# Kernel optimization log

Hardware: AMD Instinct MI355X
Metric: run time of the kernel (lower is better)

## Reference

```python
import jax, jax.numpy as jnp
import numpy as np

N, IN_F, OUT_F, H = 4096, 256, 512, 8
D = OUT_F // H  # hidden per head
NEG_SLOPE = 0.2


def setup_inputs() -> dict:
    key = jax.random.key(0)
    k1, k2, k3 = jax.random.split(key, 3)
    inp = jax.random.normal(k1, (N, IN_F), dtype=jnp.float32)
    A = jnp.zeros((N, N), dtype=jnp.float32)  # additive adjacency mask
    # xavier_uniform for W [out, in]
    limW = float(np.sqrt(6.0 / (IN_F + H * D)))
    W = jax.random.uniform(k2, (H * D, IN_F), minval=-limW, maxval=limW, dtype=jnp.float32)
    lima = float(np.sqrt(6.0 / (H * D + 1)))
    a_left = jax.random.uniform(k3, (1, H, D), minval=-lima, maxval=lima, dtype=jnp.float32)
    return {"inp": inp, "A": A, "W": W, "a_left": a_left}


def reference(inp, A, W, a_left):
    # h: [N, H, D]
    h = (inp @ W.T).reshape(-1, H, D)
    # NOTE: source uses a_left for BOTH source and target scores (a_right is dead code)
    scores = jnp.sum(h * a_left, axis=-1)  # [N, H]
    s = scores.T  # [H, N]
    # [H, N, N] additive attention logits
    logits = jax.nn.leaky_relu(s[:, :, None] + s[:, None, :], negative_slope=NEG_SLOPE)
    logits = logits + A[None, :, :]
    att = jax.nn.softmax(logits, axis=-1)  # [H, N, N]
    # bmm: [H,N,N] x [H,N,D] -> [H,N,D] -> [N,H,D]
    out = jnp.einsum('hij,jhd->ihd', att, h)
    return out.reshape(-1, H * D)
```

## Files before the change

### kernel.cpp

```cpp
#include <hip/hip_runtime.h>
#include <math.h>

#define N 4096
#define IN_F 256
#define OUT_F 512
#define H 8
#define D 64
#define NEG 0.2f
#define JC 1024

typedef __attribute__((ext_vector_type(8))) short bf16x8;
typedef __attribute__((ext_vector_type(4))) float f32x4;

__device__ __forceinline__ float leaky(float x) { return fmaxf(x, NEG * x); }

__device__ __forceinline__ unsigned short f2bf(float x) {
    union { float f; unsigned u; } v; v.f = x;
    unsigned r = v.u + 0x7fff + ((v.u >> 16) & 1);
    return (unsigned short)(r >> 16);
}

__device__ __forceinline__ unsigned fmap(float x) {
    union { float f; unsigned u; } v; v.f = x;
    return (v.u & 0x80000000u) ? ~v.u : (v.u | 0x80000000u);
}
__device__ __forceinline__ float funmap(unsigned m) {
    union { float f; unsigned u; } v;
    v.u = (m & 0x80000000u) ? (m & 0x7fffffffu) : ~m;
    return v.f;
}

__device__ __forceinline__ void dma16(const void* g, void* l) {
    __builtin_amdgcn_global_load_lds((const __attribute__((address_space(1))) void*)g,
                                     (__attribute__((address_space(3))) void*)l, 16, 0, 0);
}

__global__ __launch_bounds__(256, 4) void k_gemm(const float* __restrict__ inp,
                                                 const float* __restrict__ W,
                                                 const float* __restrict__ a_left,
                                                 unsigned short* __restrict__ hbT,
                                                 float* __restrict__ s,
                                                 unsigned* __restrict__ smaxU) {
    __shared__ float As[64][36];
    __shared__ float Bs[64][68];
    __shared__ unsigned short h_st[32][72];
    __shared__ float s_red[32];

    const int t = threadIdx.x;
    const int bi = blockIdx.x;
    const int head = blockIdx.y;
    const int iy = t >> 4, ox = t & 15;
    const int iA = t >> 3, kA = (t & 7) * 8;
    const int oB = t >> 2, kB = (t & 3) * 16;

    float4 pa[2], pb[4];
    auto loadrk = [&](int k0) {
        const float* ip = &inp[(size_t)(bi * 32 + iA) * IN_F + k0 + kA];
        const float* wp = &W[(size_t)(head * 64 + oB) * IN_F + k0 + kB];
#pragma unroll
        for (int q = 0; q < 2; ++q) pa[q] = *(const float4*)&ip[q * 4];
#pragma unroll
        for (int q = 0; q < 4; ++q) pb[q] = *(const float4*)&wp[q * 4];
    };
    loadrk(0);

    float acc[2][4] = {};
    for (int k0 = 0; k0 < IN_F; k0 += 64) {
        __syncthreads();
#pragma unroll
        for (int q = 0; q < 2; ++q)
#pragma unroll
            for (int j = 0; j < 4; ++j) As[kA + q * 4 + j][iA] = ((const float*)&pa[q])[j];
#pragma unroll
        for (int q = 0; q < 4; ++q)
#pragma unroll
            for (int j = 0; j < 4; ++j) Bs[kB + q * 4 + j][oB] = ((const float*)&pb[q])[j];
        __syncthreads();
        if (k0 + 64 < IN_F) loadrk(k0 + 64);
#pragma unroll
        for (int k = 0; k < 64; ++k) {
            float2 a2 = *(const float2*)&As[k][iy * 2];
            float4 b4 = *(const float4*)&Bs[k][ox * 4];
            float a[2] = {a2.x, a2.y};
            float b[4] = {b4.x, b4.y, b4.z, b4.w};
#pragma unroll
            for (int r = 0; r < 2; ++r)
#pragma unroll
                for (int c = 0; c < 4; ++c) acc[r][c] = fmaf(a[r], b[c], acc[r][c]);
        }
    }

    float aL[4];
#pragma unroll
    for (int c = 0; c < 4; ++c) aL[c] = a_left[head * D + ox * 4 + c];
#pragma unroll
    for (int r = 0; r < 2; ++r) {
        float sp = acc[r][0] * aL[0] + acc[r][1] * aL[1] + acc[r][2] * aL[2] + acc[r][3] * aL[3];
        sp += __shfl_xor(sp, 1); sp += __shfl_xor(sp, 2);
        sp += __shfl_xor(sp, 4); sp += __shfl_xor(sp, 8);
        if (ox == 0) {
            s[head * N + bi * 32 + iy * 2 + r] = sp;
            s_red[iy * 2 + r] = sp;
        }
    }
    __syncthreads();
    if (t < 32) {
        float m = s_red[t];
        for (int off = 16; off; off >>= 1) m = fmaxf(m, __shfl_down(m, off, 64));
        if (t == 0) atomicMax(&smaxU[head], fmap(m));
    }

#pragma unroll
    for (int r = 0; r < 2; ++r) {
        ushort4 v;
        v.x = f2bf(acc[r][0]); v.y = f2bf(acc[r][1]);
        v.z = f2bf(acc[r][2]); v.w = f2bf(acc[r][3]);
        *(ushort4*)&h_st[iy * 2 + r][ox * 4] = v;
    }
    __syncthreads();
    {
        const int d = t >> 2, iq = (t & 3) * 8;
        unsigned short us[8];
#pragma unroll
        for (int k = 0; k < 8; ++k) us[k] = h_st[iq + k][d];
        unsigned short* dst = &hbT[((size_t)(head * D + d)) * N + bi * 32 + iq];
#pragma unroll
        for (int q = 0; q < 2; ++q) {
            ushort4 v = {us[q * 4 + 0], us[q * 4 + 1], us[q * 4 + 2], us[q * 4 + 3]};
            *(ushort4*)&dst[q * 4] = v;
        }
    }
}

__global__ __launch_bounds__(256) void k_prep(const float* __restrict__ A,
                                              unsigned short* __restrict__ Abf,
                                              float* __restrict__ rmax) {
    int i = blockIdx.x;
    const float* row = &A[(size_t)i * N];
    unsigned short* dst = &Abf[(size_t)i * N];
    float m = -1e30f;
    for (int j = threadIdx.x * 4; j < N; j += 256 * 4) {
        float4 v = *(const float4*)&row[j];
        m = fmaxf(fmaxf(fmaxf(m, v.x), fmaxf(v.y, v.z)), v.w);
        ushort4 b = {f2bf(v.x), f2bf(v.y), f2bf(v.z), f2bf(v.w)};
        *(ushort4*)&dst[j] = b;
    }
    for (int off = 32; off; off >>= 1) m = fmaxf(m, __shfl_down(m, off, 64));
    __shared__ float red[4];
    if ((threadIdx.x & 63) == 0) red[threadIdx.x >> 6] = m;
    __syncthreads();
    if (threadIdx.x == 0) rmax[i] = fmaxf(fmaxf(red[0], red[1]), fmaxf(red[2], red[3]));
}

__global__ __launch_bounds__(256) void k_rowmax(const float* __restrict__ A,
                                                float* __restrict__ rmax) {
    int i = blockIdx.x;
    const float* row = &A[(size_t)i * N];
    float m = -1e30f;
    for (int j = threadIdx.x * 4; j < N; j += 256 * 4) {
        float4 v = *(const float4*)&row[j];
        m = fmaxf(fmaxf(fmaxf(m, v.x), fmaxf(v.y, v.z)), v.w);
    }
    for (int off = 32; off; off >>= 1) m = fmaxf(m, __shfl_down(m, off, 64));
    __shared__ float red[4];
    if ((threadIdx.x & 63) == 0) red[threadIdx.x >> 6] = m;
    __syncthreads();
    if (threadIdx.x == 0) rmax[i] = fmaxf(fmaxf(red[0], red[1]), fmaxf(red[2], red[3]));
}

__device__ __forceinline__ int swz(int r) { return (r ^ (r >> 2)) & 3; }

__global__ __launch_bounds__(256, 4) void k_attn_big(const unsigned short* __restrict__ Abf,
                                                     const unsigned short* __restrict__ hbT,
                                                     const float* __restrict__ s,
                                                     const unsigned* __restrict__ smaxU,
                                                     const float* __restrict__ rmax,
                                                     float* __restrict__ out,
                                                     float* __restrict__ Z) {
    __shared__ unsigned short A_st[2][128 * 32];
    __shared__ unsigned short hT_st[2][64 * 32];
    __shared__ float s_ch[JC];

    const int t = threadIdx.x;
    const int i0 = blockIdx.x * 128;
    const int head = blockIdx.y;
    const int j0 = blockIdx.z * JC;
    const int lane = t & 63, wave = t >> 6, quad = lane >> 4, li = lane & 15;

    *(float4*)&s_ch[t * 4] = *(const float4*)&s[head * N + j0 + t * 4];

    const float smx = funmap(smaxU[head]);
    float s_i[2], negmb[2];
#pragma unroll
    for (int is = 0; is < 2; ++is) {
        int row = i0 + wave * 32 + is * 16 + li;
        float sv = s[head * N + row];
        s_i[is] = sv;
        negmb[is] = -(leaky(sv + smx) + rmax[row]);
    }

    const unsigned short* gA[2]; unsigned short* lA[2][2];
#pragma unroll
    for (int q = 0; q < 2; ++q) {
        int slot = q * 256 + t, row = slot >> 2, u = slot & 3;
        gA[q] = Abf + (size_t)(i0 + row) * N + j0 + ((u ^ swz(row)) << 3);
        lA[0][q] = &A_st[0][slot * 8];
        lA[1][q] = &A_st[1][slot * 8];
    }
    const unsigned short* gH; unsigned short* lH[2];
    {
        int slot = t, d = slot >> 2, u = slot & 3;
        gH = hbT + (size_t)head * D * N + (size_t)d * N + j0 + ((u ^ swz(d)) << 3);
        lH[0] = &hT_st[0][slot * 8];
        lH[1] = &hT_st[1][slot * 8];
    }

    f32x4 acc[2][4] = {};
    f32x4 accz[2] = {};
    bf16x8 onesb;
#pragma unroll
    for (int i = 0; i < 8; ++i) onesb[i] = 0x3F80;

#pragma unroll
    for (int q = 0; q < 2; ++q) dma16(gA[q], lA[0][q]);
    dma16(gH, lH[0]);

    for (int tt = 0; tt < JC / 32; ++tt) {
        const int p = tt & 1;
        __syncthreads();
        if (tt + 1 < JC / 32) {
            const int ju = (tt + 1) * 32;
#pragma unroll
            for (int q = 0; q < 2; ++q) dma16(gA[q] + ju, lA[p ^ 1][q]);
            dma16(gH + ju, lH[p ^ 1]);
        }
        const int jt = tt * 32;

        float4 s0 = *(const float4*)&s_ch[jt + quad * 8];
        float4 s1 = *(const float4*)&s_ch[jt + quad * 8 + 4];
        float sv[8] = {s0.x, s0.y, s0.z, s0.w, s1.x, s1.y, s1.z, s1.w};
        bf16x8 hf[4];
#pragma unroll
        for (int db = 0; db < 4; ++db) {
            int d = db * 16 + li;
            hf[db] = *(const bf16x8*)&hT_st[p][(d * 4 + (quad ^ swz(d))) * 8];
        }
#pragma unroll
        for (int is = 0; is < 2; ++is) {
            int r = wave * 32 + is * 16 + li;
            uint4 au = *(const uint4*)&A_st[p][(r * 4 + (quad ^ swz(r))) * 8];
            unsigned auv[4] = {au.x, au.y, au.z, au.w};
            union { bf16x8 v; unsigned u[4]; } P;
            const float si = s_i[is], nmb = negmb[is];
#pragma unroll
            for (int w = 0; w < 4; ++w) {
                float aLo = __uint_as_float(auv[w] << 16);
                float aHi = __uint_as_float(auv[w] & 0xffff0000u);
                float t0 = si + sv[2 * w], t1 = si + sv[2 * w + 1];
                float l0 = fmaxf(t0, NEG * t0), l1 = fmaxf(t1, NEG * t1);
                float e0 = __expf(l0 + (aLo + nmb));
                float e1 = __expf(l1 + (aHi + nmb));
                unsigned r0 = __float_as_uint(e0) + 0x8000u;
                unsigned r1 = __float_as_uint(e1) + 0x8000u;
                P.u[w] = __builtin_amdgcn_perm(r1, r0, 0x07060302u);
            }
#pragma unroll
            for (int db = 0; db < 4; ++db)
                acc[is][db] = __builtin_amdgcn_mfma_f32_16x16x32_bf16(P.v, hf[db], acc[is][db], 0, 0, 0);
            accz[is] = __builtin_amdgcn_mfma_f32_16x16x32_bf16(P.v, onesb, accz[is], 0, 0, 0);
        }
    }

#pragma unroll
    for (int is = 0; is < 2; ++is) {
        int rowbase = i0 + wave * 32 + is * 16 + quad * 4;
#pragma unroll
        for (int r = 0; r < 4; ++r) {
            float* op = &out[(size_t)(rowbase + r) * OUT_F + head * D];
#pragma unroll
            for (int db = 0; db < 4; ++db) atomicAdd(&op[db * 16 + li], acc[is][db][r]);
        }
        if (li == 0) {
#pragma unroll
            for (int r = 0; r < 4; ++r) atomicAdd(&Z[head * N + rowbase + r], accz[is][r]);
        }
    }
}

#define JCF 2048
__global__ __launch_bounds__(256, 4) void k_attn_f(const float* __restrict__ A,
                                                   const unsigned short* __restrict__ hbT,
                                                   const float* __restrict__ s,
                                                   const unsigned* __restrict__ smaxU,
                                                   const float* __restrict__ rmax,
                                                   float* __restrict__ out,
                                                   float* __restrict__ Z) {
    __shared__ float A_stf[64 * 16 * 4];
    __shared__ unsigned short hT_stf[64 * 8 * 8];
    __shared__ float s_ch[JCF];

    const int t = threadIdx.x;
    const int i0 = blockIdx.x * 64;
    const int head = blockIdx.y;
    const int j0 = blockIdx.z * JCF;
    const int lane = t & 63, wave = t >> 6, quad = lane >> 4, li = lane & 15;
    const int iw = wave * 16;
    const int myrow = i0 + iw + li;

#pragma unroll
    for (int q = 0; q < 2; ++q) {
        int idx = q * 256 + t;
        *(float4*)&s_ch[idx * 4] = *(const float4*)&s[head * N + j0 + idx * 4];
    }
    const float s_i = s[head * N + myrow];
    const float mb = leaky(s_i + funmap(smaxU[head])) + rmax[myrow];

    const float* gA[4]; void* lA[4];
#pragma unroll
    for (int q = 0; q < 4; ++q) {
        int slot = q * 256 + t;
        int r = slot >> 4, c4p = slot & 15;
        int c4 = c4p ^ (r & 7);
        gA[q] = &A[(size_t)(i0 + r) * N + j0 + c4 * 4];
        lA[q] = (void*)&A_stf[slot * 4];
    }
    const unsigned short* gH[2]; void* lH[2];
#pragma unroll
    for (int q = 0; q < 2; ++q) {
        int slot = q * 256 + t;
        int r = slot >> 3, u = slot & 7;
        int uc = u ^ (r & 7);
        gH[q] = &hbT[(size_t)head * D * N + (size_t)r * N + j0 + uc * 8];
        lH[q] = (void*)&hT_stf[slot * 8];
    }

    f32x4 acc[4] = {{0, 0, 0, 0}, {0, 0, 0, 0}, {0, 0, 0, 0}, {0, 0, 0, 0}};
    float zsum = 0.f;

    for (int jt = 0; jt < JCF; jt += 64) {
        __syncthreads();
#pragma unroll
        for (int q = 0; q < 4; ++q) dma16(gA[q] + jt, lA[q]);
#pragma unroll
        for (int q = 0; q < 2; ++q) dma16(gH[q] + jt, lH[q]);
        __syncthreads();

#pragma unroll
        for (int kh = 0; kh < 2; ++kh) {
            const int u0 = kh * 8 + quad * 2;
            const int sw = li & 7;
            float4 a0 = *(const float4*)&A_stf[((iw + li) * 16 + (u0 ^ sw)) * 4];
            float4 a1 = *(const float4*)&A_stf[((iw + li) * 16 + ((u0 + 1) ^ sw)) * 4];
            const int jl = kh * 32 + quad * 8;
            float4 s0 = *(const float4*)&s_ch[jt + jl];
            float4 s1 = *(const float4*)&s_ch[jt + jl + 4];
            float av[8] = {a0.x, a0.y, a0.z, a0.w, a1.x, a1.y, a1.z, a1.w};
            float sv[8] = {s0.x, s0.y, s0.z, s0.w, s1.x, s1.y, s1.z, s1.w};
            union { bf16x8 v; unsigned u[4]; } P;
#pragma unroll
            for (int p = 0; p < 4; ++p) {
                float x0 = s_i + sv[2 * p + 0];
                float x1 = s_i + sv[2 * p + 1];
                float w0 = __expf(fmaxf(x0, NEG * x0) + (av[2 * p + 0] - mb));
                float w1 = __expf(fmaxf(x1, NEG * x1) + (av[2 * p + 1] - mb));
                zsum += w0 + w1;
                P.u[p] = ((unsigned)f2bf(w1) << 16) | (unsigned)f2bf(w0);
            }
#pragma unroll
            for (int db = 0; db < 4; ++db) {
                int slotH = (db * 16 + li) * 8 + ((kh * 4 + quad) ^ sw);
                bf16x8 hf = *(const bf16x8*)&hT_stf[slotH * 8];
                acc[db] = __builtin_amdgcn_mfma_f32_16x16x32_bf16(P.v, hf, acc[db], 0, 0, 0);
            }
        }
    }

    zsum += __shfl_xor(zsum, 16);
    zsum += __shfl_xor(zsum, 32);
    if (quad == 0) atomicAdd(&Z[head * N + myrow], zsum);

#pragma unroll
    for (int r = 0; r < 4; ++r) {
        float* op = &out[(size_t)(i0 + iw + quad * 4 + r) * OUT_F + head * D];
#pragma unroll
        for (int db = 0; db < 4; ++db) atomicAdd(&op[db * 16 + li], acc[db][r]);
    }
}

__global__ __launch_bounds__(256) void k_norm(float* __restrict__ out,
                                              const float* __restrict__ Z) {
    int idx = blockIdx.x * 256 + threadIdx.x;
    int i = idx >> 9, hd = idx & 511, hh = hd >> 6;
    out[idx] = out[idx] / Z[hh * N + i];
}

extern "C" void kernel_launch(void* const* d_in, const int* in_sizes, int n_in,
                              void* d_out, int out_size, void* d_ws, size_t ws_size,
                              hipStream_t stream) {
    const float* inp = (const float*)d_in[0];
    const float* A = (const float*)d_in[1];
    const float* W = (const float*)d_in[2];
    const float* a_left = (const float*)d_in[3];
    float* out = (float*)d_out;

    unsigned short* hbT = (unsigned short*)d_ws;
    float* s = (float*)((char*)d_ws + (size_t)H * D * N * 2);
    float* Z = s + (size_t)H * N;
    unsigned* smaxU = (unsigned*)(Z + (size_t)H * N);
    float* rmax = (float*)(smaxU + 8);
    unsigned short* Abf = (unsigned short*)((char*)d_ws + ((size_t)5 << 20));
    const bool big = ws_size >= (((size_t)5 << 20) + (size_t)N * N * 2);

    hipMemsetAsync(out, 0, (size_t)N * OUT_F * sizeof(float), stream);
    hipMemsetAsync(Z, 0, (size_t)H * N * sizeof(float) + 8 * sizeof(unsigned), stream);

    k_gemm<<<dim3(N / 32, H), 256, 0, stream>>>(inp, W, a_left, hbT, s, smaxU);
    if (big) {
        k_prep<<<dim3(N), 256, 0, stream>>>(A, Abf, rmax);
        k_attn_big<<<dim3(N / 128, H, N / JC), 256, 0, stream>>>(Abf, hbT, s, smaxU, rmax, out, Z);
    } else {
        k_rowmax<<<dim3(N), 256, 0, stream>>>(A, rmax);
        k_attn_f<<<dim3(N / 64, H, N / JCF), 256, 0, stream>>>(A, hbT, s, smaxU, rmax, out, Z);
    }
    k_norm<<<dim3(N * OUT_F / 256), 256, 0, stream>>>(out, Z);
}
```

Before: 215.3 us.

## Use split-bf16 MFMA for projection GEMM and drop LDS staging in attention

The fp32 input projection GEMM is replaced by an MFMA kernel using a hi/lo bf16 split (three MFMAs per tile) to keep near-fp32 accuracy. The split conversion of inp and W is folded into the A-prep kernel. The attention kernel drops its LDS double-buffered DMA staging and reads A and h fragments directly from global memory into registers. This trades LDS traffic and barriers for uncoalesced-ish global reads that depend on cache hits, and adds workspace for the split copies.

```diff
diff --git a/kernel.cpp b/kernel.cpp
--- a/kernel.cpp
+++ b/kernel.cpp
@@ -19,6 +19,9 @@
     unsigned r = v.u + 0x7fff + ((v.u >> 16) & 1);
     return (unsigned short)(r >> 16);
 }
+__device__ __forceinline__ float bf2f(unsigned short b) {
+    union { float f; unsigned u; } v; v.u = ((unsigned)b) << 16; return v.f;
+}
 
 __device__ __forceinline__ unsigned fmap(float x) {
     union { float f; unsigned u; } v; v.f = x;
@@ -35,12 +38,238 @@
                                      (__attribute__((address_space(3))) void*)l, 16, 0, 0);
 }
 
-__global__ __launch_bounds__(256, 4) void k_gemm(const float* __restrict__ inp,
-                                                 const float* __restrict__ W,
-                                                 const float* __restrict__ a_left,
-                                                 unsigned short* __restrict__ hbT,
-                                                 float* __restrict__ s,
-                                                 unsigned* __restrict__ smaxU) {
+
+__global__ __launch_bounds__(256) void k_prep(const float* __restrict__ A,
+                                              const float* __restrict__ inp,
+                                              const float* __restrict__ W,
+                                              unsigned short* __restrict__ Abf,
+                                              float* __restrict__ rmax,
+                                              unsigned short* __restrict__ inpH,
+                                              unsigned short* __restrict__ inpL,
+                                              unsigned short* __restrict__ WH,
+                                              unsigned short* __restrict__ WL) {
+    const int i = blockIdx.x, t = threadIdx.x;
+    const float* row = &A[(size_t)i * N];
+    unsigned short* dst = &Abf[(size_t)i * N];
+    float m = -1e30f;
+    for (int j = t * 4; j < N; j += 256 * 4) {
+        float4 v = *(const float4*)&row[j];
+        m = fmaxf(fmaxf(fmaxf(m, v.x), fmaxf(v.y, v.z)), v.w);
+        ushort4 b = {f2bf(v.x), f2bf(v.y), f2bf(v.z), f2bf(v.w)};
+        *(ushort4*)&dst[j] = b;
+    }
+    for (int off = 32; off; off >>= 1) m = fmaxf(m, __shfl_down(m, off, 64));
+    __shared__ float red[4];
+    if ((t & 63) == 0) red[t >> 6] = m;
+    __syncthreads();
+    if (t == 0) rmax[i] = fmaxf(fmaxf(red[0], red[1]), fmaxf(red[2], red[3]));
+
+    {
+        float v = inp[(size_t)i * IN_F + t];
+        unsigned short hi = f2bf(v);
+        inpH[(size_t)i * IN_F + t] = hi;
+        inpL[(size_t)i * IN_F + t] = f2bf(v - bf2f(hi));
+    }
+    if (i < OUT_F) {
+        float v = W[(size_t)i * IN_F + t];
+        unsigned short hi = f2bf(v);
+        WH[(size_t)i * IN_F + t] = hi;
+        WL[(size_t)i * IN_F + t] = f2bf(v - bf2f(hi));
+    }
+}
+
+__global__ __launch_bounds__(256) void k_gemm(const unsigned short* __restrict__ inpH,
+                                              const unsigned short* __restrict__ inpL,
+                                              const unsigned short* __restrict__ WH,
+                                              const unsigned short* __restrict__ WL,
+                                              const float* __restrict__ a_left,
+                                              unsigned short* __restrict__ hbT,
+                                              float* __restrict__ s,
+                                              unsigned* __restrict__ smaxU) {
+    __shared__ unsigned short h_st[64][72];
+    __shared__ float s_red[64];
+    const int t = threadIdx.x, bx = blockIdx.x, head = blockIdx.y;
+    const int wave = t >> 6, lane = t & 63, quad = lane >> 4, li = lane & 15;
+    const int i0 = bx * 64;
+
+    const unsigned short* pAH = inpH + (size_t)(i0 + wave * 16 + li) * IN_F + quad * 8;
+    const unsigned short* pAL = inpL + (size_t)(i0 + wave * 16 + li) * IN_F + quad * 8;
+    const unsigned short* pBH[4];
+    const unsigned short* pBL[4];
+#pragma unroll
+    for (int ot = 0; ot < 4; ++ot) {
+        pBH[ot] = WH + (size_t)(head * 64 + ot * 16 + li) * IN_F + quad * 8;
+        pBL[ot] = WL + (size_t)(head * 64 + ot * 16 + li) * IN_F + quad * 8;
+    }
+
+    f32x4 acc[4] = {};
+#pragma unroll
+    for (int ks = 0; ks < 8; ++ks) {
+        bf16x8 ah = *(const bf16x8*)(pAH + ks * 32);
+        bf16x8 al = *(const bf16x8*)(pAL + ks * 32);
+#pragma unroll
+        for (int ot = 0; ot < 4; ++ot) {
+            bf16x8 bh = *(const bf16x8*)(pBH[ot] + ks * 32);
+            bf16x8 bl = *(const bf16x8*)(pBL[ot] + ks * 32);
+            acc[ot] = __builtin_amdgcn_mfma_f32_16x16x32_bf16(ah, bh, acc[ot], 0, 0, 0);
+            acc[ot] = __builtin_amdgcn_mfma_f32_16x16x32_bf16(al, bh, acc[ot], 0, 0, 0);
+            acc[ot] = __builtin_amdgcn_mfma_f32_16x16x32_bf16(ah, bl, acc[ot], 0, 0, 0);
+        }
+    }
+
+    float aLv[4];
+#pragma unroll
+    for (int ot = 0; ot < 4; ++ot) aLv[ot] = a_left[head * D + ot * 16 + li];
+#pragma unroll
+    for (int r = 0; r < 4; ++r) {
+        float sp = acc[0][r] * aLv[0] + acc[1][r] * aLv[1] + acc[2][r] * aLv[2] + acc[3][r] * aLv[3];
+        sp += __shfl_xor(sp, 1); sp += __shfl_xor(sp, 2);
+        sp += __shfl_xor(sp, 4); sp += __shfl_xor(sp, 8);
+        if (li == 0) {
+            int rloc = wave * 16 + quad * 4 + r;
+            s[head * N + i0 + rloc] = sp;
+            s_red[rloc] = sp;
+        }
+    }
+#pragma unroll
+    for (int ot = 0; ot < 4; ++ot)
+#pragma unroll
+        for (int r = 0; r < 4; ++r)
+            h_st[wave * 16 + quad * 4 + r][ot * 16 + li] = f2bf(acc[ot][r]);
+    __syncthreads();
+    if (t < 64) {
+        float m = s_red[t];
+        for (int off = 32; off; off >>= 1) m = fmaxf(m, __shfl_down(m, off, 64));
+        if (t == 0) atomicMax(&smaxU[head], fmap(m));
+    }
+    {
+        const int d = t >> 2, iq = (t & 3) * 16;
+        unsigned short us[16];
+#pragma unroll
+        for (int k = 0; k < 16; ++k) us[k] = h_st[iq + k][d];
+        unsigned short* dst = &hbT[((size_t)(head * D + d)) * N + i0 + iq];
+#pragma unroll
+        for (int q = 0; q < 4; ++q) {
+            ushort4 v = {us[q * 4 + 0], us[q * 4 + 1], us[q * 4 + 2], us[q * 4 + 3]};
+            *(ushort4*)&dst[q * 4] = v;
+        }
+    }
+}
+
+__global__ __launch_bounds__(256, 4) void k_attn(const unsigned short* __restrict__ Abf,
+                                                 const unsigned short* __restrict__ hbT,
+                                                 const float* __restrict__ s,
+                                                 const unsigned* __restrict__ smaxU,
+                                                 const float* __restrict__ rmax,
+                                                 float* __restrict__ out,
+                                                 float* __restrict__ Z) {
+    __shared__ float s_ch[JC];
+
+    const int t = threadIdx.x;
+    const int i0 = blockIdx.x * 128;
+    const int head = blockIdx.y;
+    const int j0 = blockIdx.z * JC;
+    const int lane = t & 63, wave = t >> 6, quad = lane >> 4, li = lane & 15;
+
+    *(float4*)&s_ch[t * 4] = *(const float4*)&s[head * N + j0 + t * 4];
+
+    const float smx = funmap(smaxU[head]);
+    float s_i[2], nmb[2];
+#pragma unroll
+    for (int is = 0; is < 2; ++is) {
+        int row = i0 + wave * 32 + is * 16 + li;
+        float sv = s[head * N + row];
+        s_i[is] = sv;
+        nmb[is] = -(leaky(sv + smx) + rmax[row]);
+    }
+    __syncthreads();
+
+    const unsigned short* pA[2];
+#pragma unroll
+    for (int is = 0; is < 2; ++is)
+        pA[is] = Abf + (size_t)(i0 + wave * 32 + is * 16 + li) * N + j0 + quad * 8;
+    const unsigned short* pH[4];
+#pragma unroll
+    for (int db = 0; db < 4; ++db)
+        pH[db] = hbT + (size_t)(head * D + db * 16 + li) * N + j0 + quad * 8;
+
+    f32x4 acc[2][4] = {};
+    f32x4 accz[2] = {};
+    bf16x8 onesb;
+#pragma unroll
+    for (int i = 0; i < 8; ++i) onesb[i] = 0x3F80;
+
+    for (int tg = 0; tg < JC / 128; ++tg) {
+#pragma unroll
+        for (int u = 0; u < 4; ++u) {
+            bf16x8 hf[4];
+#pragma unroll
+            for (int db = 0; db < 4; ++db) hf[db] = *(const bf16x8*)(pH[db] + u * 32);
+            uint4 au[2];
+#pragma unroll
+            for (int is = 0; is < 2; ++is) au[is] = *(const uint4*)(pA[is] + u * 32);
+            float4 s0 = *(const float4*)&s_ch[tg * 128 + u * 32 + quad * 8];
+            float4 s1 = *(const float4*)&s_ch[tg * 128 + u * 32 + quad * 8 + 4];
+            float sv[8] = {s0.x, s0.y, s0.z, s0.w, s1.x, s1.y, s1.z, s1.w};
+#pragma unroll
+            for (int is = 0; is < 2; ++is) {
+                unsigned auv[4] = {au[is].x, au[is].y, au[is].z, au[is].w};
+                union { bf16x8 v; unsigned u[4]; } P;
+                const float si = s_i[is], nm = nmb[is];
+#pragma unroll
+                for (int w = 0; w < 4; ++w) {
+                    float aLo = __uint_as_float(auv[w] << 16);
+                    float aHi = __uint_as_float(auv[w] & 0xffff0000u);
+                    float x0 = si + sv[2 * w + 0];
+                    float x1 = si + sv[2 * w + 1];
+                    float l0 = fmaxf(x0, NEG * x0);
+                    float l1 = fmaxf(x1, NEG * x1);
+                    float e0 = __expf(l0 + (aLo + nm));
+                    float e1 = __expf(l1 + (aHi + nm));
+                    unsigned r0 = __float_as_uint(e0) + 0x8000u;
+                    unsigned r1 = __float_as_uint(e1) + 0x8000u;
+                    P.u[w] = __builtin_amdgcn_perm(r1, r0, 0x07060302u);
+                }
+#pragma unroll
+                for (int db = 0; db < 4; ++db)
+                    acc[is][db] = __builtin_amdgcn_mfma_f32_16x16x32_bf16(P.v, hf[db], acc[is][db], 0, 0, 0);
+                accz[is] = __builtin_amdgcn_mfma_f32_16x16x32_bf16(P.v, onesb, accz[is], 0, 0, 0);
+            }
+        }
+        pA[0] += 128; pA[1] += 128;
+        pH[0] += 128; pH[1] += 128; pH[2] += 128; pH[3] += 128;
+    }
+
+#pragma unroll
+    for (int is = 0; is < 2; ++is) {
+        int rowbase = i0 + wave * 32 + is * 16 + quad * 4;
+#pragma unroll
+        for (int r = 0; r < 4; ++r) {
+            float* op = &out[(size_t)(rowbase + r) * OUT_F + head * D];
+#pragma unroll
+            for (int db = 0; db < 4; ++db) atomicAdd(&op[db * 16 + li], acc[is][db][r]);
+        }
+        if (li == 0) {
+#pragma unroll
+            for (int r = 0; r < 4; ++r) atomicAdd(&Z[head * N + rowbase + r], accz[is][r]);
+        }
+    }
+}
+
+__global__ __launch_bounds__(256) void k_norm(float* __restrict__ out,
+                                              const float* __restrict__ Z) {
+    int idx = blockIdx.x * 256 + threadIdx.x;
+    int i = idx >> 9, hd = idx & 511, hh = hd >> 6;
+    out[idx] = out[idx] / Z[hh * N + i];
+}
+
+
+__global__ __launch_bounds__(256, 4) void k_gemm_f(const float* __restrict__ inp,
+                                                   const float* __restrict__ W,
+                                                   const float* __restrict__ a_left,
+                                                   unsigned short* __restrict__ hbT,
+                                                   float* __restrict__ s,
+                                                   unsigned* __restrict__ smaxU) {
     __shared__ float As[64][36];
     __shared__ float Bs[64][68];
     __shared__ unsigned short h_st[32][72];
@@ -89,7 +318,6 @@
                 for (int c = 0; c < 4; ++c) acc[r][c] = fmaf(a[r], b[c], acc[r][c]);
         }
     }
-
     float aL[4];
 #pragma unroll
     for (int c = 0; c < 4; ++c) aL[c] = a_left[head * D + ox * 4 + c];
@@ -109,7 +337,6 @@
         for (int off = 16; off; off >>= 1) m = fmaxf(m, __shfl_down(m, off, 64));
         if (t == 0) atomicMax(&smaxU[head], fmap(m));
     }
-
 #pragma unroll
     for (int r = 0; r < 2; ++r) {
         ushort4 v;
@@ -130,26 +357,6 @@
             *(ushort4*)&dst[q * 4] = v;
         }
     }
-}
-
-__global__ __launch_bounds__(256) void k_prep(const float* __restrict__ A,
-                                              unsigned short* __restrict__ Abf,
-                                              float* __restrict__ rmax) {
-    int i = blockIdx.x;
-    const float* row = &A[(size_t)i * N];
-    unsigned short* dst = &Abf[(size_t)i * N];
-    float m = -1e30f;
-    for (int j = threadIdx.x * 4; j < N; j += 256 * 4) {
-        float4 v = *(const float4*)&row[j];
-        m = fmaxf(fmaxf(fmaxf(m, v.x), fmaxf(v.y, v.z)), v.w);
-        ushort4 b = {f2bf(v.x), f2bf(v.y), f2bf(v.z), f2bf(v.w)};
-        *(ushort4*)&dst[j] = b;
-    }
-    for (int off = 32; off; off >>= 1) m = fmaxf(m, __shfl_down(m, off, 64));
-    __shared__ float red[4];
-    if ((threadIdx.x & 63) == 0) red[threadIdx.x >> 6] = m;
-    __syncthreads();
-    if (threadIdx.x == 0) rmax[i] = fmaxf(fmaxf(red[0], red[1]), fmaxf(red[2], red[3]));
 }
 
 __global__ __launch_bounds__(256) void k_rowmax(const float* __restrict__ A,
@@ -166,125 +373,6 @@
     if ((threadIdx.x & 63) == 0) red[threadIdx.x >> 6] = m;
     __syncthreads();
     if (threadIdx.x == 0) rmax[i] = fmaxf(fmaxf(red[0], red[1]), fmaxf(red[2], red[3]));
-}
-
-__device__ __forceinline__ int swz(int r) { return (r ^ (r >> 2)) & 3; }
-
-__global__ __launch_bounds__(256, 4) void k_attn_big(const unsigned short* __restrict__ Abf,
-                                                     const unsigned short* __restrict__ hbT,
-                                                     const float* __restrict__ s,
-                                                     const unsigned* __restrict__ smaxU,
-                                                     const float* __restrict__ rmax,
-                                                     float* __restrict__ out,
-                                                     float* __restrict__ Z) {
-    __shared__ unsigned short A_st[2][128 * 32];
-    __shared__ unsigned short hT_st[2][64 * 32];
-    __shared__ float s_ch[JC];
-
-    const int t = threadIdx.x;
-    const int i0 = blockIdx.x * 128;
-    const int head = blockIdx.y;
-    const int j0 = blockIdx.z * JC;
-    const int lane = t & 63, wave = t >> 6, quad = lane >> 4, li = lane & 15;
-
-    *(float4*)&s_ch[t * 4] = *(const float4*)&s[head * N + j0 + t * 4];
-
-    const float smx = funmap(smaxU[head]);
-    float s_i[2], negmb[2];
-#pragma unroll
-    for (int is = 0; is < 2; ++is) {
-        int row = i0 + wave * 32 + is * 16 + li;
-        float sv = s[head * N + row];
-        s_i[is] = sv;
-        negmb[is] = -(leaky(sv + smx) + rmax[row]);
-    }
-
-    const unsigned short* gA[2]; unsigned short* lA[2][2];
-#pragma unroll
-    for (int q = 0; q < 2; ++q) {
-        int slot = q * 256 + t, row = slot >> 2, u = slot & 3;
-        gA[q] = Abf + (size_t)(i0 + row) * N + j0 + ((u ^ swz(row)) << 3);
-        lA[0][q] = &A_st[0][slot * 8];
-        lA[1][q] = &A_st[1][slot * 8];
-    }
-    const unsigned short* gH; unsigned short* lH[2];
-    {
-        int slot = t, d = slot >> 2, u = slot & 3;
-        gH = hbT + (size_t)head * D * N + (size_t)d * N + j0 + ((u ^ swz(d)) << 3);
-        lH[0] = &hT_st[0][slot * 8];
-        lH[1] = &hT_st[1][slot * 8];
-    }
-
-    f32x4 acc[2][4] = {};
-    f32x4 accz[2] = {};
-    bf16x8 onesb;
-#pragma unroll
-    for (int i = 0; i < 8; ++i) onesb[i] = 0x3F80;
-
-#pragma unroll
-    for (int q = 0; q < 2; ++q) dma16(gA[q], lA[0][q]);
-    dma16(gH, lH[0]);
-
-    for (int tt = 0; tt < JC / 32; ++tt) {
-        const int p = tt & 1;
-        __syncthreads();
-        if (tt + 1 < JC / 32) {
-            const int ju = (tt + 1) * 32;
-#pragma unroll
-            for (int q = 0; q < 2; ++q) dma16(gA[q] + ju, lA[p ^ 1][q]);
-            dma16(gH + ju, lH[p ^ 1]);
-        }
-        const int jt = tt * 32;
-
-        float4 s0 = *(const float4*)&s_ch[jt + quad * 8];
-        float4 s1 = *(const float4*)&s_ch[jt + quad * 8 + 4];
-        float sv[8] = {s0.x, s0.y, s0.z, s0.w, s1.x, s1.y, s1.z, s1.w};
-        bf16x8 hf[4];
-#pragma unroll
-        for (int db = 0; db < 4; ++db) {
-            int d = db * 16 + li;
-            hf[db] = *(const bf16x8*)&hT_st[p][(d * 4 + (quad ^ swz(d))) * 8];
-        }
-#pragma unroll
-        for (int is = 0; is < 2; ++is) {
-            int r = wave * 32 + is * 16 + li;
-            uint4 au = *(const uint4*)&A_st[p][(r * 4 + (quad ^ swz(r))) * 8];
-            unsigned auv[4] = {au.x, au.y, au.z, au.w};
-            union { bf16x8 v; unsigned u[4]; } P;
-            const float si = s_i[is], nmb = negmb[is];
-#pragma unroll
-            for (int w = 0; w < 4; ++w) {
-                float aLo = __uint_as_float(auv[w] << 16);
-                float aHi = __uint_as_float(auv[w] & 0xffff0000u);
-                float t0 = si + sv[2 * w], t1 = si + sv[2 * w + 1];
-                float l0 = fmaxf(t0, NEG * t0), l1 = fmaxf(t1, NEG * t1);
-                float e0 = __expf(l0 + (aLo + nmb));
-                float e1 = __expf(l1 + (aHi + nmb));
-                unsigned r0 = __float_as_uint(e0) + 0x8000u;
-                unsigned r1 = __float_as_uint(e1) + 0x8000u;
-                P.u[w] = __builtin_amdgcn_perm(r1, r0, 0x07060302u);
-            }
-#pragma unroll
-            for (int db = 0; db < 4; ++db)
-                acc[is][db] = __builtin_amdgcn_mfma_f32_16x16x32_bf16(P.v, hf[db], acc[is][db], 0, 0, 0);
-            accz[is] = __builtin_amdgcn_mfma_f32_16x16x32_bf16(P.v, onesb, accz[is], 0, 0, 0);
-        }
-    }
-
-#pragma unroll
-    for (int is = 0; is < 2; ++is) {
-        int rowbase = i0 + wave * 32 + is * 16 + quad * 4;
-#pragma unroll
-        for (int r = 0; r < 4; ++r) {
-            float* op = &out[(size_t)(rowbase + r) * OUT_F + head * D];
-#pragma unroll
-            for (int db = 0; db < 4; ++db) atomicAdd(&op[db * 16 + li], acc[is][db][r]);
-        }
-        if (li == 0) {
-#pragma unroll
-            for (int r = 0; r < 4; ++r) atomicAdd(&Z[head * N + rowbase + r], accz[is][r]);
-        }
-    }
 }
 
 #define JCF 2048
@@ -387,12 +475,6 @@
     }
 }
 
-__global__ __launch_bounds__(256) void k_norm(float* __restrict__ out,
-                                              const float* __restrict__ Z) {
-    int idx = blockIdx.x * 256 + threadIdx.x;
-    int i = idx >> 9, hd = idx & 511, hh = hd >> 6;
-    out[idx] = out[idx] / Z[hh * N + i];
-}
 
 extern "C" void kernel_launch(void* const* d_in, const int* in_sizes, int n_in,
                               void* d_out, int out_size, void* d_ws, size_t ws_size,
@@ -403,22 +485,28 @@
     const float* a_left = (const float*)d_in[3];
     float* out = (float*)d_out;
 
-    unsigned short* hbT = (unsigned short*)d_ws;
-    float* s = (float*)((char*)d_ws + (size_t)H * D * N * 2);
+    char* base = (char*)d_ws;
+    unsigned short* hbT = (unsigned short*)base;
+    float* s = (float*)(base + (size_t)H * D * N * 2);
     float* Z = s + (size_t)H * N;
     unsigned* smaxU = (unsigned*)(Z + (size_t)H * N);
     float* rmax = (float*)(smaxU + 8);
-    unsigned short* Abf = (unsigned short*)((char*)d_ws + ((size_t)5 << 20));
-    const bool big = ws_size >= (((size_t)5 << 20) + (size_t)N * N * 2);
+    unsigned short* inpH = (unsigned short*)(base + ((size_t)5 << 20));
+    unsigned short* inpL = (unsigned short*)(base + ((size_t)7 << 20));
+    unsigned short* WH = (unsigned short*)(base + ((size_t)9 << 20));
+    unsigned short* WL = (unsigned short*)(base + ((size_t)9 << 20) + ((size_t)256 << 10));
+    unsigned short* Abf = (unsigned short*)(base + ((size_t)10 << 20));
+    const bool big = ws_size >= (((size_t)10 << 20) + (size_t)N * N * 2);
 
     hipMemsetAsync(out, 0, (size_t)N * OUT_F * sizeof(float), stream);
     hipMemsetAsync(Z, 0, (size_t)H * N * sizeof(float) + 8 * sizeof(unsigned), stream);
 
-    k_gemm<<<dim3(N / 32, H), 256, 0, stream>>>(inp, W, a_left, hbT, s, smaxU);
     if (big) {
-        k_prep<<<dim3(N), 256, 0, stream>>>(A, Abf, rmax);
-        k_attn_big<<<dim3(N / 128, H, N / JC), 256, 0, stream>>>(Abf, hbT, s, smaxU, rmax, out, Z);
+        k_prep<<<dim3(N), 256, 0, stream>>>(A, inp, W, Abf, rmax, inpH, inpL, WH, WL);
+        k_gemm<<<dim3(N / 64, H), 256, 0, stream>>>(inpH, inpL, WH, WL, a_left, hbT, s, smaxU);
+        k_attn<<<dim3(N / 128, H, N / JC), 256, 0, stream>>>(Abf, hbT, s, smaxU, rmax, out, Z);
     } else {
+        k_gemm_f<<<dim3(N / 32, H), 256, 0, stream>>>(inp, W, a_left, hbT, s, smaxU);
         k_rowmax<<<dim3(N), 256, 0, stream>>>(A, rmax);
         k_attn_f<<<dim3(N / 64, H, N / JCF), 256, 0, stream>>>(A, hbT, s, smaxU, rmax, out, Z);
     }
```

New measurement: 250.6 us. 16.4% more time.
